# Kernel optimization log

Hardware: AMD Instinct MI355X
Metric: run time of the kernel (lower is better)

The kernel has to match this reference:

```python
import jax, jax.numpy as jnp
import numpy as np

NE = 50000   # num edges (nodes of the line graph)
NA = 800000  # adjacency pairs in the edge graph (~avg degree 16)
NC = 100000  # triadic candidates
F = 64       # edge_feat_dim
H = 128      # hidden_dim
L = 3        # num_layers


def setup_inputs() -> dict:
    key = jax.random.key(0)
    ks = iter(jax.random.split(key, 32))

    def w(shape, scale=0.05):
        return jax.random.normal(next(ks), shape, dtype=jnp.float32) * scale

    inp = {
        "edge_features": jax.random.normal(next(ks), (NE, F), dtype=jnp.float32),
        "adj_dst": jnp.sort(jax.random.randint(next(ks), (NA,), 0, NE)),
        "adj_src": jax.random.randint(next(ks), (NA,), 0, NE),
        "cand_i": jax.random.randint(next(ks), (NC,), 0, NE),
        "cand_j": jax.random.randint(next(ks), (NC,), 0, NE),
        # edge encoder: Linear(F,H) -> ReLU -> Linear(H,H)
        "enc_W1": w((F, H)), "enc_b1": jnp.zeros((H,), jnp.float32),
        "enc_W2": w((H, H)), "enc_b2": jnp.zeros((H,), jnp.float32),
        # per-layer message_net: Linear(2H,H) -> ReLU -> Linear(H,H)
        "msg_W1": w((L, 2 * H, H)), "msg_b1": jnp.zeros((L, H), jnp.float32),
        "msg_W2": w((L, H, H)), "msg_b2": jnp.zeros((L, H), jnp.float32),
        # per-layer update_net: Linear(2H,H) -> ReLU -> Linear(H,H)
        "upd_W1": w((L, 2 * H, H)), "upd_b1": jnp.zeros((L, H), jnp.float32),
        "upd_W2": w((L, H, H)), "upd_b2": jnp.zeros((L, H), jnp.float32),
        # triadic predictor: Linear(2H,H)->ReLU->Linear(H,H)->ReLU->Linear(H,1)
        "pred_W1": w((2 * H, H)), "pred_b1": jnp.zeros((H,), jnp.float32),
        "pred_W2": w((H, H)), "pred_b2": jnp.zeros((H,), jnp.float32),
        "pred_W3": w((H, 1)), "pred_b3": jnp.zeros((1,), jnp.float32),
    }
    return inp


def _mlp2(x, W1, b1, W2, b2):
    return jnp.maximum(x @ W1 + b1, 0.0) @ W2 + b2


def reference(edge_features, adj_dst, adj_src, cand_i, cand_j,
              enc_W1, enc_b1, enc_W2, enc_b2,
              msg_W1, msg_b1, msg_W2, msg_b2,
              upd_W1, upd_b1, upd_W2, upd_b2,
              pred_W1, pred_b1, pred_W2, pred_b2, pred_W3, pred_b3):
    # encode edge features -> [NE, H]
    e = _mlp2(edge_features, enc_W1, enc_b1, enc_W2, enc_b2)

    # degree of each edge-node in the line graph
    deg = jax.ops.segment_sum(jnp.ones((adj_dst.shape[0],), e.dtype), adj_dst,
                              num_segments=NE)  # [NE]
    inv_deg = 1.0 / jnp.maximum(deg, 1.0)
    isolated = (deg == 0.0)[:, None]

    for l in range(L):
        # per-pair message: message_net(concat(e_i, e_j))
        pair = jnp.concatenate([e[adj_dst], e[adj_src]], axis=-1)  # [NA, 2H]
        msgs = _mlp2(pair, msg_W1[l], msg_b1[l], msg_W2[l], msg_b2[l])  # [NA, H]
        agg = jax.ops.segment_sum(msgs, adj_dst, num_segments=NE) * inv_deg[:, None]
        # edges with no neighbors: message_net(concat(e_i, e_i))
        self_msg = _mlp2(jnp.concatenate([e, e], axis=-1),
                         msg_W1[l], msg_b1[l], msg_W2[l], msg_b2[l])
        message = jnp.where(isolated, self_msg, agg)
        # update: update_net(concat(e_i, message_i)), then outer ReLU
        e = _mlp2(jnp.concatenate([e, message], axis=-1),
                  upd_W1[l], upd_b1[l], upd_W2[l], upd_b2[l])
        e = jnp.maximum(e, 0.0)

    # triadic predictor on parent-edge pairs (dropout inactive at eval)
    comb = jnp.concatenate([e[cand_i], e[cand_j]], axis=-1)  # [NC, 2H]
    h = jnp.maximum(comb @ pred_W1 + pred_b1, 0.0)
    h = jnp.maximum(h @ pred_W2 + pred_b2, 0.0)
    logits = (h @ pred_W3 + pred_b3)[:, 0]  # [NC]
    probs = jax.nn.sigmoid(logits)
    return probs, logits
```

## Files before the change

### kernel.cpp

```cpp
#include <hip/hip_runtime.h>
#include <hip/hip_bf16.h>

#define NE 50000
#define NA 800000
#define NC 100000

typedef _Float16 f16;
typedef f16 half8 __attribute__((ext_vector_type(8)));
typedef f16 f16x2 __attribute__((ext_vector_type(2)));
typedef float f32x4 __attribute__((ext_vector_type(4)));

#define OFF_ENC1 0
#define OFF_ENC2 8192
#define OFF_MSGPQ 24576
#define OFF_UPD1 122880
#define OFF_UPD2 221184
#define OFF_PREDPQ 270336
#define OFF_PREDW2 303104
#define TOTAL_WT 319488

#define R_FUSE 49536
#define R_WT 270336
#define R_X 800000
#define R_Z 50000
#define PTOT (R_FUSE + R_WT + R_X + R_Z)

struct KP {
    const float* edge_features;
    const int *adj_dst, *adj_src, *cand_i, *cand_j;
    const float *enc_b1, *enc_b2;
    const float *msg_b1, *msg_W2, *msg_b2;
    const float *upd_W1, *upd_b1, *upd_b2;
    const float *pred_b1, *pred_b2, *pred_W3, *pred_b3;
    f16* wt;
    float* fbias;
    f16 *xb, *eA, *eB, *P0, *Q0, *P1, *Q1;
    int *segStart, *segEnd;
    float *outP, *outL;
    const float* wsrc[20];
    int wK[20], wOff[20], wStr[20], wCum[21];
};


__device__ __forceinline__ void prep_item(const KP& p, int gid) {
    if (gid < R_FUSE) {
        int g = gid >> 7, n = gid & 127;
        int l = g / 129, kk = g % 129;
        const float* U1b = p.upd_W1 + (size_t)l * 32768 + 16384;
        if (kk < 128) {
            const float* w2row = p.msg_W2 + (size_t)l * 16384 + (size_t)kk * 128;
            float s = 0.f;
            for (int m = 0; m < 128; ++m) s += w2row[m] * U1b[m * 128 + n];
            p.wt[OFF_UPD1 + l * 32768 + n * 256 + 128 + kk] = (f16)s;
        } else {
            const float* b2 = p.msg_b2 + l * 128;
            float s = p.upd_b1[l * 128 + n];
            for (int m = 0; m < 128; ++m) s += b2[m] * U1b[m * 128 + n];
            p.fbias[l * 128 + n] = s;
        }
    } else if (gid < R_FUSE + R_WT) {
        int e = gid - R_FUSE;
        int j = 0;
#pragma unroll
        for (int i = 1; i < 20; ++i) j += (e >= p.wCum[i]) ? 1 : 0;
        int r = e - p.wCum[j];
        int K = p.wK[j];
        int k = r % K, n = r / K;
        p.wt[p.wOff[j] + n * p.wStr[j] + k] = (f16)p.wsrc[j][(size_t)k * 128 + n];
    } else if (gid < R_FUSE + R_WT + R_X) {
        int g2 = gid - (R_FUSE + R_WT);
        float4 v = ((const float4*)p.edge_features)[g2];
        f16x2 a = {(f16)v.x, (f16)v.y}, b = {(f16)v.z, (f16)v.w};
        ((f16x2*)p.xb)[g2 * 2] = a;
        ((f16x2*)p.xb)[g2 * 2 + 1] = b;
    } else if (gid < PTOT) {
        int z = gid - (R_FUSE + R_WT + R_X);
        p.segStart[z] = 0;
        p.segEnd[z] = 0;
    }
}

__device__ __forceinline__ void degseg_item(const KP& p, int i) {
    int d = p.adj_dst[i];
    if (i == 0 || p.adj_dst[i - 1] != d) p.segStart[d] = i;
    if (i == NA - 1 || p.adj_dst[i + 1] != d) p.segEnd[d] = i + 1;
}

template <int K1, int MR, bool AGG>
__device__ __forceinline__ void do_tile(
    char* SMEM, f16* gscr, int tile, const f16* __restrict__ in0,
    const f16* __restrict__ Pin, const f16* __restrict__ Qin,
    const int* __restrict__ adj_src, const int* __restrict__ segStart,
    const int* __restrict__ segEnd,
    const f16* __restrict__ w1t, const int w1s, const float* __restrict__ b1v,
    const f16* __restrict__ w2t, const float* __restrict__ b2v, const bool reluOut,
    f16* __restrict__ oute,
    const f16* __restrict__ wpq, const float* __restrict__ bPp,
    f16* __restrict__ Pout, f16* __restrict__ Qout) {
    constexpr int SA = K1 + 8;
    constexpr int SH = 136;
    constexpr int MT = MR / 16;
    f16* Abuf = (f16*)SMEM;
    f16* Hbuf = (f16*)SMEM;
    f16* Ebuf = (f16*)(SMEM + MR * SH * 2);
    const int t = threadIdx.x, lane = t & 63, wave = t >> 6;
    const int quad = lane >> 4, mn = lane & 15, n0 = wave * 32;
    const int rbase = tile * MR;

    if constexpr (K1 == 64) {
#pragma unroll
        for (int it = 0; it < (MR * 8) / 256; ++it) {
            int u = it * 256 + t, row = u >> 3, k = (u & 7) * 8, gr = rbase + row;
            half8 v = {};
            if (gr < NE) v = *(const half8*)(in0 + (size_t)gr * 64 + k);
            *(half8*)(Abuf + row * SA + k) = v;
        }
    } else {
#pragma unroll
        for (int it = 0; it < (MR * 16) / 256; ++it) {
            int u = it * 256 + t, row = u >> 4, k = (u & 15) * 8, gr = rbase + row;
            half8 v = {};
            if (gr < NE) v = *(const half8*)(in0 + (size_t)gr * 128 + k);
            *(half8*)(Abuf + row * SA + k) = v;
        }
    }
    if constexpr (AGG) {
        const int waveU = __builtin_amdgcn_readfirstlane(wave);
        f16* wscr = gscr + waveU * 4096;
        int par = 0;
        for (int i = 0; i < MR / 4; ++i) {
            int drow = waveU * (MR / 4) + i;
            int dst = rbase + drow;
            if (dst >= NE) break;
            int s = segStart[dst];
            int deg = segEnd[dst] - s;
            f16x2 p2 = ((const f16x2*)Pin)[(size_t)dst * 64 + lane];
            float p0 = (float)p2.x, p1 = (float)p2.y;
            float x0 = 0.f, x1 = 0.f;
            if (deg == 0) {
                f16x2 q2 = ((const f16x2*)Qin)[(size_t)dst * 64 + lane];
                x0 = fmaxf(p0 + (float)q2.x, 0.f);
                x1 = fmaxf(p1 + (float)q2.y, 0.f);
            } else {
                for (int base = 0; base < deg; base += 16) {
                    int cnt = deg - base;
                    cnt = cnt < 16 ? cnt : 16;
                    int ia = s + base + (lane & 15);
                    ia = ia < NA - 1 ? ia : NA - 1;
                    int idxv = adj_src[ia];
                    f16* buf = wscr + (par & 1) * 2048;
                    par++;
                    __builtin_amdgcn_s_waitcnt(0xc07f);
                    for (int j = 0; j < cnt; ++j) {
                        int sj = __shfl(idxv, j, 64);
                        const f16* gp = Qin + (size_t)sj * 128 + lane * 2;
                        __builtin_amdgcn_global_load_lds(
                            (const __attribute__((address_space(1))) void*)gp,
                            (__attribute__((address_space(3))) void*)(buf + j * 128),
                            4, 0, 0);
                    }
                    __builtin_amdgcn_s_waitcnt(0x0f70);
                    for (int j = 0; j < cnt; ++j) {
                        f16x2 q2 = *(const f16x2*)(buf + j * 128 + lane * 2);
                        x0 += fmaxf(p0 + (float)q2.x, 0.f);
                        x1 += fmaxf(p1 + (float)q2.y, 0.f);
                    }
                }
                float sc = 1.f / (float)deg;
                x0 *= sc;
                x1 *= sc;
            }
            f16x2 o = {(f16)x0, (f16)x1};
            *(f16x2*)(Abuf + drow * SA + 128 + lane * 2) = o;
        }
    }
    __syncthreads();

    f32x4 acc[MT][2];
    {
        float bb0 = b1v[n0 + mn], bb1 = b1v[n0 + 16 + mn];
#pragma unroll
        for (int mt = 0; mt < MT; ++mt) {
            acc[mt][0] = (f32x4){bb0, bb0, bb0, bb0};
            acc[mt][1] = (f32x4){bb1, bb1, bb1, bb1};
        }
    }
#pragma unroll
    for (int kc = 0; kc < K1 / 32; ++kc) {
        half8 wA = *(const half8*)(w1t + (size_t)(n0 + mn) * w1s + kc * 32 + quad * 8);
        half8 wB = *(const half8*)(w1t + (size_t)(n0 + 16 + mn) * w1s + kc * 32 + quad * 8);
        half8 af[MT];
#pragma unroll
        for (int mt = 0; mt < MT; ++mt)
            af[mt] = *(const half8*)(Abuf + (mt * 16 + mn) * SA + kc * 32 + quad * 8);
#pragma unroll
        for (int mt = 0; mt < MT; ++mt) {
            acc[mt][0] = __builtin_amdgcn_mfma_f32_16x16x32_f16(af[mt], wA, acc[mt][0], 0, 0, 0);
            acc[mt][1] = __builtin_amdgcn_mfma_f32_16x16x32_f16(af[mt], wB, acc[mt][1], 0, 0, 0);
        }
    }
    __syncthreads();
#pragma unroll
    for (int mt = 0; mt < MT; ++mt)
#pragma unroll
        for (int nt = 0; nt < 2; ++nt)
#pragma unroll
            for (int r = 0; r < 4; ++r)
                Hbuf[(mt * 16 + quad * 4 + r) * SH + n0 + nt * 16 + mn] =
                    (f16)fmaxf(acc[mt][nt][r], 0.f);
    __syncthreads();

    {
        float bb0 = b2v[n0 + mn], bb1 = b2v[n0 + 16 + mn];
#pragma unroll
        for (int mt = 0; mt < MT; ++mt) {
            acc[mt][0] = (f32x4){bb0, bb0, bb0, bb0};
            acc[mt][1] = (f32x4){bb1, bb1, bb1, bb1};
        }
    }
#pragma unroll
    for (int kc = 0; kc < 4; ++kc) {
        half8 wA = *(const half8*)(w2t + (size_t)(n0 + mn) * 128 + kc * 32 + quad * 8);
        half8 wB = *(const half8*)(w2t + (size_t)(n0 + 16 + mn) * 128 + kc * 32 + quad * 8);
        half8 af[MT];
#pragma unroll
        for (int mt = 0; mt < MT; ++mt)
            af[mt] = *(const half8*)(Hbuf + (mt * 16 + mn) * SH + kc * 32 + quad * 8);
#pragma unroll
        for (int mt = 0; mt < MT; ++mt) {
            acc[mt][0] = __builtin_amdgcn_mfma_f32_16x16x32_f16(af[mt], wA, acc[mt][0], 0, 0, 0);
            acc[mt][1] = __builtin_amdgcn_mfma_f32_16x16x32_f16(af[mt], wB, acc[mt][1], 0, 0, 0);
        }
    }
#pragma unroll
    for (int mt = 0; mt < MT; ++mt)
#pragma unroll
        for (int nt = 0; nt < 2; ++nt)
#pragma unroll
            for (int r = 0; r < 4; ++r) {
                float v = acc[mt][nt][r];
                if (reluOut) v = fmaxf(v, 0.f);
                Ebuf[(mt * 16 + quad * 4 + r) * SH + n0 + nt * 16 + mn] = (f16)v;
            }
    __syncthreads();

#pragma unroll
    for (int it = 0; it < (MR * 16) / 256; ++it) {
        int u = it * 256 + t, row = u >> 4, k = (u & 15) * 8, gr = rbase + row;
        if (gr < NE) {
            half8 v = *(const half8*)(Ebuf + row * SH + k);
            *(half8*)(oute + (size_t)gr * 128 + k) = v;
        }
    }

    {
        float bb0 = bPp[n0 + mn], bb1 = bPp[n0 + 16 + mn];
#pragma unroll
        for (int mt = 0; mt < MT; ++mt) {
            acc[mt][0] = (f32x4){bb0, bb0, bb0, bb0};
            acc[mt][1] = (f32x4){bb1, bb1, bb1, bb1};
        }
    }
#pragma unroll
    for (int kc = 0; kc < 4; ++kc) {
        half8 wA = *(const half8*)(wpq + (size_t)(n0 + mn) * 128 + kc * 32 + quad * 8);
        half8 wB = *(const half8*)(wpq + (size_t)(n0 + 16 + mn) * 128 + kc * 32 + quad * 8);
        half8 af[MT];
#pragma unroll
        for (int mt = 0; mt < MT; ++mt)
            af[mt] = *(const half8*)(Ebuf + (mt * 16 + mn) * SH + kc * 32 + quad * 8);
#pragma unroll
        for (int mt = 0; mt < MT; ++mt) {
            acc[mt][0] = __builtin_amdgcn_mfma_f32_16x16x32_f16(af[mt], wA, acc[mt][0], 0, 0, 0);
            acc[mt][1] = __builtin_amdgcn_mfma_f32_16x16x32_f16(af[mt], wB, acc[mt][1], 0, 0, 0);
        }
    }
#pragma unroll
    for (int mt = 0; mt < MT; ++mt)
#pragma unroll
        for (int nt = 0; nt < 2; ++nt)
#pragma unroll
            for (int r = 0; r < 4; ++r) {
                int gr = rbase + mt * 16 + quad * 4 + r;
                if (gr < NE)
                    Pout[(size_t)gr * 128 + n0 + nt * 16 + mn] = (f16)acc[mt][nt][r];
            }
#pragma unroll
    for (int mt = 0; mt < MT; ++mt) {
        acc[mt][0] = (f32x4){0.f, 0.f, 0.f, 0.f};
        acc[mt][1] = (f32x4){0.f, 0.f, 0.f, 0.f};
    }
#pragma unroll
    for (int kc = 0; kc < 4; ++kc) {
        half8 wA = *(const half8*)(wpq + 16384 + (size_t)(n0 + mn) * 128 + kc * 32 + quad * 8);
        half8 wB = *(const half8*)(wpq + 16384 + (size_t)(n0 + 16 + mn) * 128 + kc * 32 + quad * 8);
        half8 af[MT];
#pragma unroll
        for (int mt = 0; mt < MT; ++mt)
            af[mt] = *(const half8*)(Ebuf + (mt * 16 + mn) * SH + kc * 32 + quad * 8);
#pragma unroll
        for (int mt = 0; mt < MT; ++mt) {
            acc[mt][0] = __builtin_amdgcn_mfma_f32_16x16x32_f16(af[mt], wA, acc[mt][0], 0, 0, 0);
            acc[mt][1] = __builtin_amdgcn_mfma_f32_16x16x32_f16(af[mt], wB, acc[mt][1], 0, 0, 0);
        }
    }
#pragma unroll
    for (int mt = 0; mt < MT; ++mt)
#pragma unroll
        for (int nt = 0; nt < 2; ++nt)
#pragma unroll
            for (int r = 0; r < 4; ++r) {
                int gr = rbase + mt * 16 + quad * 4 + r;
                if (gr < NE)
                    Qout[(size_t)gr * 128 + n0 + nt * 16 + mn] = (f16)acc[mt][nt][r];
            }
}

__device__ __forceinline__ void pred_tile(const KP& p, char* SMEM, float* w3s,
                                          float* psum, int tile, float b3v) {
    constexpr int SA = 136, SO = 133;
    f16* Abuf = (f16*)SMEM;
    float* Obuf = (float*)SMEM;
    const int t = threadIdx.x, lane = t & 63, wave = t >> 6;
    const int quad = lane >> 4, mn = lane & 15, n0 = wave * 32;
    const int rbase = tile << 6;
#pragma unroll
    for (int it = 0; it < 4; ++it) {
        int u = it * 256 + t, row = u >> 4, k = (u & 15) * 8, gr = rbase + row;
        half8 v = {};
        if (gr < NC) {
            int ii = p.cand_i[gr], jj = p.cand_j[gr];
            half8 a = *(const half8*)(p.P1 + (size_t)ii * 128 + k);
            half8 b = *(const half8*)(p.Q1 + (size_t)jj * 128 + k);
#pragma unroll
            for (int x = 0; x < 8; ++x)
                v[x] = (f16)fmaxf((float)a[x] + (float)b[x], 0.f);
        }
        *(half8*)(Abuf + row * SA + k) = v;
    }
    __syncthreads();
    f32x4 acc[4][2];
    {
        float bb0 = p.pred_b2[n0 + mn], bb1 = p.pred_b2[n0 + 16 + mn];
#pragma unroll
        for (int mt = 0; mt < 4; ++mt) {
            acc[mt][0] = (f32x4){bb0, bb0, bb0, bb0};
            acc[mt][1] = (f32x4){bb1, bb1, bb1, bb1};
        }
    }
#pragma unroll
    for (int kc = 0; kc < 4; ++kc) {
        half8 wA = *(const half8*)(p.wt + OFF_PREDW2 + (size_t)(n0 + mn) * 128 + kc * 32 + quad * 8);
        half8 wB = *(const half8*)(p.wt + OFF_PREDW2 + (size_t)(n0 + 16 + mn) * 128 + kc * 32 + quad * 8);
        half8 af[4];
#pragma unroll
        for (int mt = 0; mt < 4; ++mt)
            af[mt] = *(const half8*)(Abuf + (mt * 16 + mn) * SA + kc * 32 + quad * 8);
#pragma unroll
        for (int mt = 0; mt < 4; ++mt) {
            acc[mt][0] = __builtin_amdgcn_mfma_f32_16x16x32_f16(af[mt], wA, acc[mt][0], 0, 0, 0);
            acc[mt][1] = __builtin_amdgcn_mfma_f32_16x16x32_f16(af[mt], wB, acc[mt][1], 0, 0, 0);
        }
    }
    __syncthreads();
#pragma unroll
    for (int mt = 0; mt < 4; ++mt)
#pragma unroll
        for (int nt = 0; nt < 2; ++nt)
#pragma unroll
            for (int r = 0; r < 4; ++r)
                Obuf[(mt * 16 + quad * 4 + r) * SO + n0 + nt * 16 + mn] =
                    fmaxf(acc[mt][nt][r], 0.f);
    __syncthreads();
    {
        int row = t & 63, q4 = t >> 6;
        float s = 0.f;
#pragma unroll
        for (int i = 0; i < 32; ++i)
            s += Obuf[row * SO + q4 * 32 + i] * w3s[q4 * 32 + i];
        psum[t] = s;
    }
    __syncthreads();
    if (t < 64) {
        int gr = rbase + t;
        if (gr < NC) {
            float lg = psum[t] + psum[t + 64] + psum[t + 128] + psum[t + 192] + b3v;
            p.outL[gr] = lg;
            p.outP[gr] = 1.f / (1.f + expf(-lg));
        }
    }
}

__device__ __forceinline__ void upd_layer_ptrs(const KP& p, int l,
    const f16*& ein, f16*& eout, const f16*& Pin, const f16*& Qin,
    f16*& Pout, f16*& Qout, const f16*& wpq, const float*& bP) {
    ein = (l & 1) ? p.eB : p.eA;
    eout = (l & 1) ? p.eA : p.eB;
    Pin = (l & 1) ? p.P1 : p.P0;
    Qin = (l & 1) ? p.Q1 : p.Q0;
    Pout = (l & 1) ? p.P0 : p.P1;
    Qout = (l & 1) ? p.Q0 : p.Q1;
    wpq = (l < 2) ? (p.wt + OFF_MSGPQ + (l + 1) * 32768) : (p.wt + OFF_PREDPQ);
    bP = (l < 2) ? (p.msg_b1 + (l + 1) * 128) : p.pred_b1;
}

__global__ void k_prep(KP p) {
    int gid = blockIdx.x * 256 + threadIdx.x;
    if (gid < PTOT) prep_item(p, gid);
}
__global__ __launch_bounds__(256, 2) void k_encdeg(KP p) {
    __shared__ __align__(16) char SMEM[34816];
    do_tile<64, 64, false>(SMEM, nullptr, blockIdx.x, p.xb, nullptr, nullptr, nullptr, nullptr,
                           nullptr, p.wt + OFF_ENC1, 64, p.enc_b1, p.wt + OFF_ENC2, p.enc_b2,
                           false, p.eA, p.wt + OFF_MSGPQ, p.msg_b1, p.P0, p.Q0);
    const int nthr = gridDim.x * 256;
    for (int i = blockIdx.x * 256 + threadIdx.x; i < NA; i += nthr) degseg_item(p, i);
}
__global__ __launch_bounds__(256, 2) void k_upd(KP p, int l) {
    __shared__ __align__(16) char SMEM[17408];
    __shared__ __align__(16) f16 GSCR[16384];
    const f16 *ein, *Pin, *Qin, *wpq;
    f16 *eout, *Pout, *Qout;
    const float* bP;
    upd_layer_ptrs(p, l, ein, eout, Pin, Qin, Pout, Qout, wpq, bP);
    do_tile<256, 32, true>(SMEM, GSCR, blockIdx.x, ein, Pin, Qin, p.adj_src, p.segStart,
                           p.segEnd, p.wt + OFF_UPD1 + l * 32768, 256, p.fbias + l * 128,
                           p.wt + OFF_UPD2 + l * 16384, p.upd_b2 + l * 128, true,
                           eout, wpq, bP, Pout, Qout);
}
__global__ __launch_bounds__(256, 2) void k_pred(KP p) {
    __shared__ __align__(16) char SMEM[34816];
    __shared__ float w3s[128];
    __shared__ float psum[256];
    if (threadIdx.x < 128) w3s[threadIdx.x] = p.pred_W3[threadIdx.x];
    float b3v = p.pred_b3[0];
    pred_tile(p, SMEM, w3s, psum, blockIdx.x, b3v);
}

extern "C" void kernel_launch(void* const* d_in, const int* in_sizes, int n_in,
                              void* d_out, int out_size, void* d_ws, size_t ws_size,
                              hipStream_t stream) {
    KP p;
    p.edge_features = (const float*)d_in[0];
    p.adj_dst = (const int*)d_in[1];
    p.adj_src = (const int*)d_in[2];
    p.cand_i = (const int*)d_in[3];
    p.cand_j = (const int*)d_in[4];
    const float* enc_W1 = (const float*)d_in[5];
    p.enc_b1 = (const float*)d_in[6];
    const float* enc_W2 = (const float*)d_in[7];
    p.enc_b2 = (const float*)d_in[8];
    const float* msg_W1 = (const float*)d_in[9];
    p.msg_b1 = (const float*)d_in[10];
    p.msg_W2 = (const float*)d_in[11];
    p.msg_b2 = (const float*)d_in[12];
    p.upd_W1 = (const float*)d_in[13];
    p.upd_b1 = (const float*)d_in[14];
    const float* upd_W2 = (const float*)d_in[15];
    p.upd_b2 = (const float*)d_in[16];
    const float* pred_W1 = (const float*)d_in[17];
    p.pred_b1 = (const float*)d_in[18];
    const float* pred_W2 = (const float*)d_in[19];
    p.pred_b2 = (const float*)d_in[20];
    p.pred_W3 = (const float*)d_in[21];
    p.pred_b3 = (const float*)d_in[22];

    char* ws = (char*)d_ws;
    size_t off = 0;
    auto alloc = [&](size_t bytes) -> void* {
        void* q = ws + off;
        off = (off + bytes + 255) & ~(size_t)255;
        return q;
    };
    p.wt = (f16*)alloc((size_t)TOTAL_WT * 2);
    p.fbias = (float*)alloc(3 * 128 * 4);
    p.xb = (f16*)alloc((size_t)NE * 64 * 2);
    p.eA = (f16*)alloc((size_t)NE * 128 * 2);
    p.eB = (f16*)alloc((size_t)NE * 128 * 2);
    p.P0 = (f16*)alloc((size_t)NE * 128 * 2);
    p.Q0 = (f16*)alloc((size_t)NE * 128 * 2);
    p.P1 = (f16*)alloc((size_t)NE * 128 * 2);
    p.Q1 = (f16*)alloc((size_t)NE * 128 * 2);
    p.segStart = (int*)alloc((size_t)NE * 4);
    p.segEnd = (int*)alloc((size_t)NE * 4);
    p.outP = (float*)d_out;
    p.outL = (float*)d_out + NC;

    int idx = 0, c = 0;
    auto addj = [&](const float* s, int K, int o, int st) {
        p.wsrc[idx] = s; p.wK[idx] = K; p.wOff[idx] = o;
        p.wStr[idx] = st; p.wCum[idx] = c;
        c += K * 128; idx++;
    };
    addj(enc_W1, 64, OFF_ENC1, 64);
    addj(enc_W2, 128, OFF_ENC2, 128);
    for (int l = 0; l < 3; ++l) addj(msg_W1 + (size_t)l * 32768, 128, OFF_MSGPQ + l * 32768, 128);
    for (int l = 0; l < 3; ++l) addj(msg_W1 + (size_t)l * 32768 + 16384, 128, OFF_MSGPQ + l * 32768 + 16384, 128);
    for (int l = 0; l < 3; ++l) addj(p.upd_W1 + (size_t)l * 32768, 128, OFF_UPD1 + l * 32768, 256);
    for (int l = 0; l < 3; ++l) addj(upd_W2 + (size_t)l * 16384, 128, OFF_UPD2 + l * 16384, 128);
    addj(pred_W1, 128, OFF_PREDPQ, 128);
    addj(pred_W1 + 16384, 128, OFF_PREDPQ + 16384, 128);
    addj(pred_W2, 128, OFF_PREDW2, 128);
    for (int i = idx; i <= 20; ++i) p.wCum[i] = c;

    const int tilesNE64 = (NE + 63) / 64;
    const int tilesNE32 = (NE + 31) / 32;
    const int tilesNC = (NC + 63) / 64;
    k_prep<<<(PTOT + 255) / 256, 256, 0, stream>>>(p);
    k_encdeg<<<tilesNE64, 256, 0, stream>>>(p);
    for (int l = 0; l < 3; ++l) k_upd<<<tilesNE32, 256, 0, stream>>>(p, l);
    k_pred<<<tilesNC, 256, 0, stream>>>(p);

    (void)in_sizes; (void)n_in; (void)out_size; (void)ws_size;
}
```

Baseline: 466.2 us.

## Stream wave edge ranges through CSR rowptr with double-buffered neighbor gathers

Replaces the separate segStart/segEnd arrays with a single CSR rowptr, built without a zero-init pass. Each wave now walks its destinations' contiguous edge range as one stream. Source indices are batched 128 at a time into LDS, and the 16-row Q gathers are double-buffered so the next batch loads while the current one accumulates. P rows for the tile are staged in LDS up front. This targets per-destination gather latency and the tail waste when a degree is not a multiple of 16, at the cost of more LDS, a more complex control loop, and the rowptr fill loop running sequentially per element.

Measured after the change: 557.3 us. 19.5% more time.

```diff
diff --git a/kernel.cpp b/kernel.cpp
--- a/kernel.cpp
+++ b/kernel.cpp
@@ -9,6 +9,9 @@
 typedef f16 half8 __attribute__((ext_vector_type(8)));
 typedef f16 f16x2 __attribute__((ext_vector_type(2)));
 typedef float f32x4 __attribute__((ext_vector_type(4)));
+
+#define AS1 __attribute__((address_space(1)))
+#define AS3 __attribute__((address_space(3)))
 
 #define OFF_ENC1 0
 #define OFF_ENC2 8192
@@ -22,8 +25,7 @@
 #define R_FUSE 49536
 #define R_WT 270336
 #define R_X 800000
-#define R_Z 50000
-#define PTOT (R_FUSE + R_WT + R_X + R_Z)
+#define PTOT (R_FUSE + R_WT + R_X)
 
 struct KP {
     const float* edge_features;
@@ -35,7 +37,7 @@
     f16* wt;
     float* fbias;
     f16 *xb, *eA, *eB, *P0, *Q0, *P1, *Q1;
-    int *segStart, *segEnd;
+    int* rowptr;
     float *outP, *outL;
     const float* wsrc[20];
     int wK[20], wOff[20], wStr[20], wCum[21];
@@ -67,31 +69,28 @@
         int K = p.wK[j];
         int k = r % K, n = r / K;
         p.wt[p.wOff[j] + n * p.wStr[j] + k] = (f16)p.wsrc[j][(size_t)k * 128 + n];
-    } else if (gid < R_FUSE + R_WT + R_X) {
+    } else if (gid < PTOT) {
         int g2 = gid - (R_FUSE + R_WT);
         float4 v = ((const float4*)p.edge_features)[g2];
         f16x2 a = {(f16)v.x, (f16)v.y}, b = {(f16)v.z, (f16)v.w};
         ((f16x2*)p.xb)[g2 * 2] = a;
         ((f16x2*)p.xb)[g2 * 2 + 1] = b;
-    } else if (gid < PTOT) {
-        int z = gid - (R_FUSE + R_WT + R_X);
-        p.segStart[z] = 0;
-        p.segEnd[z] = 0;
-    }
-}
-
-__device__ __forceinline__ void degseg_item(const KP& p, int i) {
+    }
+}
+
+__device__ __forceinline__ void rowptr_item(const KP& p, int i) {
     int d = p.adj_dst[i];
-    if (i == 0 || p.adj_dst[i - 1] != d) p.segStart[d] = i;
-    if (i == NA - 1 || p.adj_dst[i + 1] != d) p.segEnd[d] = i + 1;
+    int prev = (i == 0) ? -1 : p.adj_dst[i - 1];
+    for (int dd = prev + 1; dd <= d; ++dd) p.rowptr[dd] = i;
+    if (i == NA - 1)
+        for (int dd = d + 1; dd <= NE; ++dd) p.rowptr[dd] = NA;
 }
 
 template <int K1, int MR, bool AGG>
 __device__ __forceinline__ void do_tile(
-    char* SMEM, f16* gscr, int tile, const f16* __restrict__ in0,
+    char* SMEM, f16* gscr, f16* pbuf, int tile, const f16* __restrict__ in0,
     const f16* __restrict__ Pin, const f16* __restrict__ Qin,
-    const int* __restrict__ adj_src, const int* __restrict__ segStart,
-    const int* __restrict__ segEnd,
+    const int* __restrict__ adj_src, const int* __restrict__ rowptr,
     const f16* __restrict__ w1t, const int w1s, const float* __restrict__ b1v,
     const f16* __restrict__ w2t, const float* __restrict__ b2v, const bool reluOut,
     f16* __restrict__ oute,
@@ -100,6 +99,7 @@
     constexpr int SA = K1 + 8;
     constexpr int SH = 136;
     constexpr int MT = MR / 16;
+    constexpr int DPW = MR / 4;
     f16* Abuf = (f16*)SMEM;
     f16* Hbuf = (f16*)SMEM;
     f16* Ebuf = (f16*)(SMEM + MR * SH * 2);
@@ -125,53 +125,134 @@
         }
     }
     if constexpr (AGG) {
+#pragma unroll
+        for (int it = 0; it < (MR * 16) / 256; ++it) {
+            int u = it * 256 + t, row = u >> 4, k = (u & 15) * 8, gr = rbase + row;
+            half8 v = {};
+            if (gr < NE) v = *(const half8*)(Pin + (size_t)gr * 128 + k);
+            *(half8*)(pbuf + row * 128 + k) = v;
+        }
+        __syncthreads();
         const int waveU = __builtin_amdgcn_readfirstlane(wave);
-        f16* wscr = gscr + waveU * 4096;
-        int par = 0;
-        for (int i = 0; i < MR / 4; ++i) {
-            int drow = waveU * (MR / 4) + i;
-            int dst = rbase + drow;
-            if (dst >= NE) break;
-            int s = segStart[dst];
-            int deg = segEnd[dst] - s;
-            f16x2 p2 = ((const f16x2*)Pin)[(size_t)dst * 64 + lane];
-            float p0 = (float)p2.x, p1 = (float)p2.y;
-            float x0 = 0.f, x1 = 0.f;
-            if (deg == 0) {
-                f16x2 q2 = ((const f16x2*)Qin)[(size_t)dst * 64 + lane];
-                x0 = fmaxf(p0 + (float)q2.x, 0.f);
-                x1 = fmaxf(p1 + (float)q2.y, 0.f);
-            } else {
-                for (int base = 0; base < deg; base += 16) {
-                    int cnt = deg - base;
-                    cnt = cnt < 16 ? cnt : 16;
-                    int ia = s + base + (lane & 15);
-                    ia = ia < NA - 1 ? ia : NA - 1;
-                    int idxv = adj_src[ia];
-                    f16* buf = wscr + (par & 1) * 2048;
-                    par++;
-                    __builtin_amdgcn_s_waitcnt(0xc07f);
-                    for (int j = 0; j < cnt; ++j) {
+        f16* rows = gscr + waveU * 4352;
+        int* idxb = (int*)(rows + 4096);
+        int d0 = rbase + waveU * DPW;
+        int dmax = NE - d0;
+        if (dmax > DPW) dmax = DPW;
+        if (dmax > 0) {
+            int bnd[DPW + 1];
+#pragma unroll
+            for (int k = 0; k <= DPW; ++k) {
+                int dd = d0 + k;
+                if (dd > NE) dd = NE;
+                bnd[k] = __builtin_amdgcn_readfirstlane(rowptr[dd]);
+            }
+            const int eBeg = bnd[0], eEnd = bnd[dmax];
+            float p0, p1, x0 = 0.f, x1 = 0.f;
+            int kcur = 0;
+            {
+                f16x2 pp = *(const f16x2*)(pbuf + (waveU * DPW) * 128 + lane * 2);
+                p0 = (float)pp.x;
+                p1 = (float)pp.y;
+            }
+            int ecur = eBeg;
+            for (int cb = eBeg; cb < eEnd; cb += 128) {
+                int cN = eEnd - cb;
+                if (cN > 128) cN = 128;
+                {
+                    int ia = cb + lane;
+                    if (ia > eEnd - 1) ia = eEnd - 1;
+                    __builtin_amdgcn_global_load_lds((const AS1 void*)(adj_src + ia),
+                                                     (AS3 void*)idxb, 4, 0, 0);
+                    int ia2 = cb + 64 + lane;
+                    if (ia2 > eEnd - 1) ia2 = eEnd - 1;
+                    __builtin_amdgcn_global_load_lds((const AS1 void*)(adj_src + ia2),
+                                                     (AS3 void*)(idxb + 64), 4, 0, 0);
+                    __builtin_amdgcn_s_waitcnt(0x0f70);
+                }
+                int nb = (cN + 15) >> 4;
+                {
+                    int idxv = idxb[mn];
+#pragma unroll
+                    for (int j = 0; j < 16; ++j) {
                         int sj = __shfl(idxv, j, 64);
-                        const f16* gp = Qin + (size_t)sj * 128 + lane * 2;
                         __builtin_amdgcn_global_load_lds(
-                            (const __attribute__((address_space(1))) void*)gp,
-                            (__attribute__((address_space(3))) void*)(buf + j * 128),
-                            4, 0, 0);
+                            (const AS1 void*)(Qin + (size_t)sj * 128 + lane * 2),
+                            (AS3 void*)(rows + j * 128), 4, 0, 0);
                     }
-                    __builtin_amdgcn_s_waitcnt(0x0f70);
-                    for (int j = 0; j < cnt; ++j) {
+                }
+                for (int b = 0; b < nb; ++b) {
+                    if (b + 1 < nb) {
+                        int idxv = idxb[(b + 1) * 16 + mn];
+                        f16* nbuf = rows + ((b + 1) & 1) * 2048;
+#pragma unroll
+                        for (int j = 0; j < 16; ++j) {
+                            int sj = __shfl(idxv, j, 64);
+                            __builtin_amdgcn_global_load_lds(
+                                (const AS1 void*)(Qin + (size_t)sj * 128 + lane * 2),
+                                (AS3 void*)(nbuf + j * 128), 4, 0, 0);
+                        }
+                        __builtin_amdgcn_s_waitcnt(0x4f70);
+                    } else {
+                        __builtin_amdgcn_s_waitcnt(0x0f70);
+                    }
+                    int m = cN - b * 16;
+                    if (m > 16) m = 16;
+                    f16* buf = rows + (b & 1) * 2048;
+                    for (int j = 0; j < m; ++j) {
+                        while (kcur < dmax && ecur >= bnd[kcur + 1]) {
+                            int deg = bnd[kcur + 1] - bnd[kcur];
+                            float r0, r1;
+                            if (deg > 0) {
+                                float sc = 1.f / (float)deg;
+                                r0 = x0 * sc;
+                                r1 = x1 * sc;
+                            } else {
+                                f16x2 q2 = ((const f16x2*)Qin)[(size_t)(d0 + kcur) * 64 + lane];
+                                r0 = fmaxf(p0 + (float)q2.x, 0.f);
+                                r1 = fmaxf(p1 + (float)q2.y, 0.f);
+                            }
+                            f16x2 o = {(f16)r0, (f16)r1};
+                            *(f16x2*)(Abuf + (waveU * DPW + kcur) * SA + 128 + lane * 2) = o;
+                            x0 = 0.f;
+                            x1 = 0.f;
+                            ++kcur;
+                            if (kcur < dmax) {
+                                f16x2 pp = *(const f16x2*)(pbuf + (waveU * DPW + kcur) * 128 + lane * 2);
+                                p0 = (float)pp.x;
+                                p1 = (float)pp.y;
+                            }
+                        }
                         f16x2 q2 = *(const f16x2*)(buf + j * 128 + lane * 2);
                         x0 += fmaxf(p0 + (float)q2.x, 0.f);
                         x1 += fmaxf(p1 + (float)q2.y, 0.f);
+                        ++ecur;
                     }
                 }
-                float sc = 1.f / (float)deg;
-                x0 *= sc;
-                x1 *= sc;
-            }
-            f16x2 o = {(f16)x0, (f16)x1};
-            *(f16x2*)(Abuf + drow * SA + 128 + lane * 2) = o;
+            }
+            while (kcur < dmax) {
+                int deg = bnd[kcur + 1] - bnd[kcur];
+                float r0, r1;
+                if (deg > 0) {
+                    float sc = 1.f / (float)deg;
+                    r0 = x0 * sc;
+                    r1 = x1 * sc;
+                } else {
+                    f16x2 q2 = ((const f16x2*)Qin)[(size_t)(d0 + kcur) * 64 + lane];
+                    r0 = fmaxf(p0 + (float)q2.x, 0.f);
+                    r1 = fmaxf(p1 + (float)q2.y, 0.f);
+                }
+                f16x2 o = {(f16)r0, (f16)r1};
+                *(f16x2*)(Abuf + (waveU * DPW + kcur) * SA + 128 + lane * 2) = o;
+                x0 = 0.f;
+                x1 = 0.f;
+                ++kcur;
+                if (kcur < dmax) {
+                    f16x2 pp = *(const f16x2*)(pbuf + (waveU * DPW + kcur) * 128 + lane * 2);
+                    p0 = (float)pp.x;
+                    p1 = (float)pp.y;
+                }
+            }
         }
     }
     __syncthreads();
@@ -410,21 +491,23 @@
 }
 __global__ __launch_bounds__(256, 2) void k_encdeg(KP p) {
     __shared__ __align__(16) char SMEM[34816];
-    do_tile<64, 64, false>(SMEM, nullptr, blockIdx.x, p.xb, nullptr, nullptr, nullptr, nullptr,
-                           nullptr, p.wt + OFF_ENC1, 64, p.enc_b1, p.wt + OFF_ENC2, p.enc_b2,
-                           false, p.eA, p.wt + OFF_MSGPQ, p.msg_b1, p.P0, p.Q0);
+    do_tile<64, 64, false>(SMEM, nullptr, nullptr, blockIdx.x, p.xb, nullptr, nullptr,
+                           nullptr, nullptr, p.wt + OFF_ENC1, 64, p.enc_b1,
+                           p.wt + OFF_ENC2, p.enc_b2, false, p.eA,
+                           p.wt + OFF_MSGPQ, p.msg_b1, p.P0, p.Q0);
     const int nthr = gridDim.x * 256;
-    for (int i = blockIdx.x * 256 + threadIdx.x; i < NA; i += nthr) degseg_item(p, i);
+    for (int i = blockIdx.x * 256 + threadIdx.x; i < NA; i += nthr) rowptr_item(p, i);
 }
 __global__ __launch_bounds__(256, 2) void k_upd(KP p, int l) {
     __shared__ __align__(16) char SMEM[17408];
-    __shared__ __align__(16) f16 GSCR[16384];
+    __shared__ __align__(16) f16 GSCR[4 * 4352];
+    __shared__ __align__(16) f16 PBUF[32 * 128];
     const f16 *ein, *Pin, *Qin, *wpq;
     f16 *eout, *Pout, *Qout;
     const float* bP;
     upd_layer_ptrs(p, l, ein, eout, Pin, Qin, Pout, Qout, wpq, bP);
-    do_tile<256, 32, true>(SMEM, GSCR, blockIdx.x, ein, Pin, Qin, p.adj_src, p.segStart,
-                           p.segEnd, p.wt + OFF_UPD1 + l * 32768, 256, p.fbias + l * 128,
+    do_tile<256, 32, true>(SMEM, GSCR, PBUF, blockIdx.x, ein, Pin, Qin, p.adj_src,
+                           p.rowptr, p.wt + OFF_UPD1 + l * 32768, 256, p.fbias + l * 128,
                            p.wt + OFF_UPD2 + l * 16384, p.upd_b2 + l * 128, true,
                            eout, wpq, bP, Pout, Qout);
 }
@@ -481,8 +564,7 @@
     p.Q0 = (f16*)alloc((size_t)NE * 128 * 2);
     p.P1 = (f16*)alloc((size_t)NE * 128 * 2);
     p.Q1 = (f16*)alloc((size_t)NE * 128 * 2);
-    p.segStart = (int*)alloc((size_t)NE * 4);
-    p.segEnd = (int*)alloc((size_t)NE * 4);
+    p.rowptr = (int*)alloc((size_t)(NE + 1) * 4);
     p.outP = (float*)d_out;
     p.outL = (float*)d_out + NC;
 
```
